# Optimization experiments

Measured on AMD Instinct MI355X. Metric: run time of the kernel, lower is better.

The kernel has to match this reference:

```python
import jax, jax.numpy as jnp
import numpy as np

S = 32            # state_size
K = 26            # neighbors
N_LOCAL, N_FUNC = 3, 14
DT = 0.3          # CNF Euler step size
CNF_STEPS = 3
GATE_H = 8


def _layernorm(x, g, b, eps=1e-5):
    mu = jnp.mean(x, axis=-1, keepdims=True)
    var = jnp.mean((x - mu) ** 2, axis=-1, keepdims=True)
    return (x - mu) * jax.lax.rsqrt(var + eps) * g + b


def setup_inputs() -> dict:
    key = jax.random.key(0)
    ks = jax.random.split(key, 16)
    B = 65536
    def w(k, shape, scale=0.1):
        return jax.random.normal(k, shape, dtype=jnp.float32) * scale
    return {
        "current_state": jax.random.normal(ks[0], (B, S), dtype=jnp.float32),
        "neighbor_states": jax.random.normal(ks[1], (B, K, S), dtype=jnp.float32),
        # local expert (SimpleLinear): [state, mean(local_nb)] -> state
        "Wl": w(ks[2], (2 * S, S)), "bl": jnp.zeros((S,), jnp.float32),
        # functional expert (hybrid GNN + CNF)
        "Wm": w(ks[3], (S, S)), "bm": jnp.zeros((S,), jnp.float32),
        "Wu": w(ks[4], (2 * S, S)), "bu": jnp.zeros((S,), jnp.float32),
        "Wc": w(ks[5], (S, S)), "bc": jnp.zeros((S,), jnp.float32),
        # distant expert (lightweight CNF)
        "Wd": w(ks[6], (2 * S, S)), "bd": jnp.zeros((S,), jnp.float32),
        # gating network
        "ln_g": jnp.ones((S,), jnp.float32), "ln_b": jnp.zeros((S,), jnp.float32),
        "gW1": w(ks[7], (2 * S, GATE_H)), "gb1": jnp.zeros((GATE_H,), jnp.float32),
        "gW2": w(ks[8], (GATE_H, 3)), "gb2": jnp.zeros((3,), jnp.float32),
    }


def reference(current_state, neighbor_states, Wl, bl, Wm, bm, Wu, bu, Wc, bc,
              Wd, bd, ln_g, ln_b, gW1, gb1, gW2, gb2):
    x = current_state                                   # [B, S]
    # --- tier classification (static slices per connection_ratios) ---
    nb_local = neighbor_states[:, :N_LOCAL]             # [B, 3, S]
    nb_func = neighbor_states[:, N_LOCAL:N_LOCAL + N_FUNC]  # [B, 14, S]
    nb_dist = neighbor_states[:, N_LOCAL + N_FUNC:]     # [B, 9, S]

    # --- local expert: simple linear on [state, mean(local neighbors)] ---
    loc_agg = jnp.mean(nb_local, axis=1)
    y_local = x + jnp.tanh(jnp.concatenate([x, loc_agg], -1) @ Wl + bl)

    # --- functional expert: GNN message passing + one CNF Euler step ---
    msgs = jax.nn.gelu(nb_func @ Wm + bm)               # [B, 14, S]
    agg = jnp.mean(msgs, axis=1)                        # [B, S]
    h = x + jnp.tanh(jnp.concatenate([x, agg], -1) @ Wu + bu)
    y_func = h + DT * jnp.tanh(h @ Wc + bc)

    # --- distant expert: lightweight CNF (Euler integration) ---
    dist_agg = jnp.mean(nb_dist, axis=1)                # [B, S]
    xt = x
    for _ in range(CNF_STEPS):
        xt = xt + DT * jnp.tanh(jnp.concatenate([xt, dist_agg], -1) @ Wd + bd)
    y_dist = xt

    # --- gating network (exact GatingNetwork math) ---
    neighbor_activity = jnp.mean(jnp.abs(neighbor_states), axis=1)  # [B, S]
    ctx = jnp.concatenate([_layernorm(x, ln_g, ln_b), neighbor_activity], -1)
    gate = jax.nn.softmax(jax.nn.gelu(ctx @ gW1 + gb1) @ gW2 + gb2, axis=-1)  # [B, 3]

    stacked = jnp.stack([y_local, y_func, y_dist], axis=1)  # [B, 3, S]
    combined = jnp.sum(stacked * gate[..., None], axis=1)   # [B, S]
    return combined, gate
```

## Files before the change

kernel.cpp:

```cpp
#include <hip/hip_runtime.h>

typedef float f32x4 __attribute__((ext_vector_type(4)));
typedef __bf16 bf16x8 __attribute__((ext_vector_type(8)));
typedef unsigned short ushort8 __attribute__((ext_vector_type(8)));

#define S 32
#define DTC 0.3f

__device__ __forceinline__ float frcp(float x) { return __builtin_amdgcn_rcpf(x); }

__device__ __forceinline__ float ftanh(float x) {
    float e = __expf(2.0f * x);
    return 1.0f - 2.0f * frcp(e + 1.0f);
}

__device__ __forceinline__ float fgelu(float x) {
    float t = ftanh(0.7978845608028654f * x * (1.0f + 0.044715f * x * x));
    return 0.5f * x * (1.0f + t);
}

__device__ __forceinline__ unsigned short f2bf(float f) {
    unsigned int u = __builtin_bit_cast(unsigned int, f);
    u += 0x7fffu + ((u >> 16) & 1u);
    return (unsigned short)(u >> 16);
}

union ABFrag { ushort8 u; bf16x8 v; };

__device__ __forceinline__ void load_row8(const float* p, float out[8]) {
    const float4* q = reinterpret_cast<const float4*>(p);
    float4 a = q[0], b = q[1];
    out[0]=a.x; out[1]=a.y; out[2]=a.z; out[3]=a.w;
    out[4]=b.x; out[5]=b.y; out[6]=b.z; out[7]=b.w;
}

__device__ __forceinline__ ABFrag pack8(const float f[8]) {
    ABFrag r;
    #pragma unroll
    for (int e = 0; e < 8; e++) r.u[e] = f2bf(f[e]);
    return r;
}

__device__ __forceinline__ ABFrag load_w(const float* W, int kbase, int col) {
    ABFrag r;
    #pragma unroll
    for (int e = 0; e < 8; e++) r.u[e] = f2bf(W[(kbase + e) * S + col]);
    return r;
}

#define MFMA(a, b, c) __builtin_amdgcn_mfma_f32_16x16x32_bf16((a), (b), (c), 0, 0, 0)

#define BOUNCE(dstFrag, srcC, scale)                                            \
    {                                                                           \
        _Pragma("unroll")                                                       \
        for (int nt_ = 0; nt_ < 2; nt_++)                                       \
            _Pragma("unroll")                                                   \
            for (int r_ = 0; r_ < 4; r_++)                                      \
                lbuf[wid][(4*lg + r_)*40 + lr + 16*nt_] =                       \
                    f2bf((srcC)[nt_][r_] * (scale));                            \
        __syncthreads();                                                        \
        (dstFrag).u = *(const ushort8*)&lbuf[wid][lr*40 + 8*lg];                \
        __syncthreads();                                                        \
    }

__global__ __launch_bounds__(256, 1) void moe_kernel(
    const float* __restrict__ cs,  const float* __restrict__ nb,
    const float* __restrict__ Wl,  const float* __restrict__ bl,
    const float* __restrict__ Wm,  const float* __restrict__ bm,
    const float* __restrict__ Wu,  const float* __restrict__ bu,
    const float* __restrict__ Wc,  const float* __restrict__ bc,
    const float* __restrict__ Wd,  const float* __restrict__ bd,
    const float* __restrict__ lng, const float* __restrict__ lnb,
    const float* __restrict__ gW1, const float* __restrict__ gb1,
    const float* __restrict__ gW2, const float* __restrict__ gb2,
    float* __restrict__ out, int B)
{
    __shared__ __align__(16) unsigned short lbuf[4][16 * 40];
    __shared__ float gbuf[4][16][4];

    const int tid = threadIdx.x;
    const int wid = tid >> 6, lane = tid & 63;
    const int lr = lane & 15, lg = lane >> 4;
    const int b0 = (blockIdx.x * 4 + wid) * 16;
    if (b0 >= B) return;

    ABFrag WlB[2][2], WuB[2][2], WdB[2][2], WmB[2], WcB[2];
    #pragma unroll
    for (int nt = 0; nt < 2; nt++) {
        const int col = lr + 16 * nt;
        #pragma unroll
        for (int kt = 0; kt < 2; kt++) {
            WlB[kt][nt] = load_w(Wl, kt * 32 + 8 * lg, col);
            WuB[kt][nt] = load_w(Wu, kt * 32 + 8 * lg, col);
            WdB[kt][nt] = load_w(Wd, kt * 32 + 8 * lg, col);
        }
        WmB[nt] = load_w(Wm, 8 * lg, col);
        WcB[nt] = load_w(Wc, 8 * lg, col);
    }
    const float blc[2] = { bl[lr], bl[lr + 16] };
    const float bmc[2] = { bm[lr], bm[lr + 16] };
    const float buc[2] = { bu[lr], bu[lr + 16] };
    const float bcc[2] = { bc[lr], bc[lr + 16] };
    const float bdc[2] = { bd[lr], bd[lr + 16] };

    float xf[8];
    load_row8(cs + (size_t)(b0 + lr) * S + 8 * lg, xf);
    ABFrag xA = pack8(xf);
    float xC[2][4];
    #pragma unroll
    for (int nt = 0; nt < 2; nt++)
        #pragma unroll
        for (int r = 0; r < 4; r++)
            xC[nt][r] = cs[(size_t)(b0 + 4 * lg + r) * S + lr + 16 * nt];

    float act[8];
    #pragma unroll
    for (int e = 0; e < 8; e++) act[e] = 0.0f;

    float locf[8];
    #pragma unroll
    for (int e = 0; e < 8; e++) locf[e] = 0.0f;
    #pragma unroll
    for (int k = 0; k < 3; k++) {
        float rf[8];
        load_row8(nb + ((size_t)(b0 + lr) * 26 + k) * S + 8 * lg, rf);
        #pragma unroll
        for (int e = 0; e < 8; e++) { locf[e] += rf[e]; act[e] += fabsf(rf[e]); }
    }
    #pragma unroll
    for (int e = 0; e < 8; e++) locf[e] *= (1.0f / 3.0f);
    ABFrag locA = pack8(locf);

    float ylC[2][4];
    #pragma unroll
    for (int nt = 0; nt < 2; nt++) {
        f32x4 acc = { blc[nt], blc[nt], blc[nt], blc[nt] };
        acc = MFMA(xA.v,   WlB[0][nt].v, acc);
        acc = MFMA(locA.v, WlB[1][nt].v, acc);
        #pragma unroll
        for (int r = 0; r < 4; r++) ylC[nt][r] = xC[nt][r] + ftanh(acc[r]);
    }

    float aggC[2][4];
    #pragma unroll
    for (int nt = 0; nt < 2; nt++)
        #pragma unroll
        for (int r = 0; r < 4; r++) aggC[nt][r] = 0.0f;
    #pragma unroll 2
    for (int k = 0; k < 14; k++) {
        float rf[8];
        load_row8(nb + ((size_t)(b0 + lr) * 26 + 3 + k) * S + 8 * lg, rf);
        #pragma unroll
        for (int e = 0; e < 8; e++) act[e] += fabsf(rf[e]);
        ABFrag a = pack8(rf);
        #pragma unroll
        for (int nt = 0; nt < 2; nt++) {
            f32x4 am = { bmc[nt], bmc[nt], bmc[nt], bmc[nt] };
            am = MFMA(a.v, WmB[nt].v, am);
            #pragma unroll
            for (int r = 0; r < 4; r++) aggC[nt][r] += fgelu(am[r]);
        }
    }

    ABFrag aggA;
    BOUNCE(aggA, aggC, (1.0f / 14.0f));

    float hC[2][4], yfC[2][4];
    #pragma unroll
    for (int nt = 0; nt < 2; nt++) {
        f32x4 acc = { buc[nt], buc[nt], buc[nt], buc[nt] };
        acc = MFMA(xA.v,   WuB[0][nt].v, acc);
        acc = MFMA(aggA.v, WuB[1][nt].v, acc);
        #pragma unroll
        for (int r = 0; r < 4; r++) hC[nt][r] = xC[nt][r] + ftanh(acc[r]);
    }
    ABFrag hA;
    BOUNCE(hA, hC, 1.0f);
    #pragma unroll
    for (int nt = 0; nt < 2; nt++) {
        f32x4 acc = { bcc[nt], bcc[nt], bcc[nt], bcc[nt] };
        acc = MFMA(hA.v, WcB[nt].v, acc);
        #pragma unroll
        for (int r = 0; r < 4; r++) yfC[nt][r] = hC[nt][r] + DTC * ftanh(acc[r]);
    }

    float distf[8];
    #pragma unroll
    for (int e = 0; e < 8; e++) distf[e] = 0.0f;
    #pragma unroll 3
    for (int k = 0; k < 9; k++) {
        float rf[8];
        load_row8(nb + ((size_t)(b0 + lr) * 26 + 17 + k) * S + 8 * lg, rf);
        #pragma unroll
        for (int e = 0; e < 8; e++) { distf[e] += rf[e]; act[e] += fabsf(rf[e]); }
    }
    #pragma unroll
    for (int e = 0; e < 8; e++) distf[e] *= (1.0f / 9.0f);
    ABFrag distA = pack8(distf);

    {
        float s = 0.0f;
        #pragma unroll
        for (int e = 0; e < 8; e++) s += xf[e];
        s += __shfl_xor(s, 16); s += __shfl_xor(s, 32);
        const float mu = s * (1.0f / S);
        float v = 0.0f;
        #pragma unroll
        for (int e = 0; e < 8; e++) { float d = xf[e] - mu; v += d * d; }
        v += __shfl_xor(v, 16); v += __shfl_xor(v, 32);
        const float rstd = rsqrtf(v * (1.0f / S) + 1e-5f);

        float g1v[8];
        #pragma unroll
        for (int u = 0; u < 8; u++) g1v[u] = 0.0f;
        #pragma unroll
        for (int e = 0; e < 8; e++) {
            const int i = 8 * lg + e;
            const float a  = (xf[e] - mu) * rstd * lng[i] + lnb[i];
            const float ac = act[e] * (1.0f / 26.0f);
            #pragma unroll
            for (int u = 0; u < 8; u++)
                g1v[u] += a * gW1[i * 8 + u] + ac * gW1[(S + i) * 8 + u];
        }
        float l0 = gb2[0], l1 = gb2[1], l2 = gb2[2];
        #pragma unroll
        for (int u = 0; u < 8; u++) {
            float gt = g1v[u];
            gt += __shfl_xor(gt, 16); gt += __shfl_xor(gt, 32);
            const float g = fgelu(gt + gb1[u]);
            l0 += g * gW2[u * 3 + 0];
            l1 += g * gW2[u * 3 + 1];
            l2 += g * gW2[u * 3 + 2];
        }
        const float mx = fmaxf(l0, fmaxf(l1, l2));
        const float e0 = __expf(l0 - mx), e1 = __expf(l1 - mx), e2 = __expf(l2 - mx);
        const float rs = frcp(e0 + e1 + e2);
        if (lg == 0) {
            gbuf[wid][lr][0] = e0 * rs;
            gbuf[wid][lr][1] = e1 * rs;
            gbuf[wid][lr][2] = e2 * rs;
        }
    }
    __syncthreads();

    float xtC[2][4];
    #pragma unroll
    for (int nt = 0; nt < 2; nt++)
        #pragma unroll
        for (int r = 0; r < 4; r++) xtC[nt][r] = xC[nt][r];
    ABFrag xtA = xA;
    #pragma unroll 1
    for (int it = 0; it < 3; it++) {
        #pragma unroll
        for (int nt = 0; nt < 2; nt++) {
            f32x4 acc = { bdc[nt], bdc[nt], bdc[nt], bdc[nt] };
            acc = MFMA(xtA.v,  WdB[0][nt].v, acc);
            acc = MFMA(distA.v, WdB[1][nt].v, acc);
            #pragma unroll
            for (int r = 0; r < 4; r++) xtC[nt][r] += DTC * ftanh(acc[r]);
        }
        if (it < 2) { BOUNCE(xtA, xtC, 1.0f); }
    }

    #pragma unroll
    for (int nt = 0; nt < 2; nt++)
        #pragma unroll
        for (int r = 0; r < 4; r++) {
            const int brow = 4 * lg + r;
            const float g0 = gbuf[wid][brow][0];
            const float g1 = gbuf[wid][brow][1];
            const float g2 = gbuf[wid][brow][2];
            out[(size_t)(b0 + brow) * S + lr + 16 * nt] =
                g0 * ylC[nt][r] + g1 * yfC[nt][r] + g2 * xtC[nt][r];
        }
    if (lg == 0) {
        float* gp = out + (size_t)B * S + (size_t)(b0 + lr) * 3;
        gp[0] = gbuf[wid][lr][0];
        gp[1] = gbuf[wid][lr][1];
        gp[2] = gbuf[wid][lr][2];
    }
}

extern "C" void kernel_launch(void* const* d_in, const int* in_sizes, int n_in,
                              void* d_out, int out_size, void* d_ws, size_t ws_size,
                              hipStream_t stream)
{
    const int B = in_sizes[0] / S;
    dim3 block(256);
    dim3 grid((B + 63) / 64);
    hipLaunchKernelGGL(moe_kernel, grid, block, 0, stream,
        (const float*)d_in[0],  (const float*)d_in[1],
        (const float*)d_in[2],  (const float*)d_in[3],
        (const float*)d_in[4],  (const float*)d_in[5],
        (const float*)d_in[6],  (const float*)d_in[7],
        (const float*)d_in[8],  (const float*)d_in[9],
        (const float*)d_in[10], (const float*)d_in[11],
        (const float*)d_in[12], (const float*)d_in[13],
        (const float*)d_in[14], (const float*)d_in[15],
        (const float*)d_in[16], (const float*)d_in[17],
        (float*)d_out, B);
}
```

Baseline: 56.07 us.

## Replace block barriers with wave-local LDS fences and use native bf16 conversion

Each wave only touches its own slice of the LDS bounce and gate buffers, so the block-wide __syncthreads calls become an s_waitcnt lgkmcnt(0) plus a compiler reorder fence. The aim is to stop the four waves stalling on each other. Manual round-to-nearest bf16 packing is replaced by native __bf16 casts. Launch bounds are raised to allow two blocks per CU, and the layernorm and gate weights are now loaded as float4 vectors instead of scalars. The main risk is correctness: this relies on wave-synchronous LDS visibility, and the compiler could reorder LDS accesses around the inline-asm fences.

```diff
diff --git a/kernel.cpp b/kernel.cpp
--- a/kernel.cpp
+++ b/kernel.cpp
@@ -2,7 +2,6 @@
 
 typedef float f32x4 __attribute__((ext_vector_type(4)));
 typedef __bf16 bf16x8 __attribute__((ext_vector_type(8)));
-typedef unsigned short ushort8 __attribute__((ext_vector_type(8)));
 
 #define S 32
 #define DTC 0.3f
@@ -19,13 +18,10 @@
     return 0.5f * x * (1.0f + t);
 }
 
-__device__ __forceinline__ unsigned short f2bf(float f) {
-    unsigned int u = __builtin_bit_cast(unsigned int, f);
-    u += 0x7fffu + ((u >> 16) & 1u);
-    return (unsigned short)(u >> 16);
-}
-
-union ABFrag { ushort8 u; bf16x8 v; };
+#define WAVE_LDS_FENCE() asm volatile("s_waitcnt lgkmcnt(0)" ::: "memory")
+#define REORDER_FENCE()  asm volatile("" ::: "memory")
+
+union ABFrag { bf16x8 v; };
 
 __device__ __forceinline__ void load_row8(const float* p, float out[8]) {
     const float4* q = reinterpret_cast<const float4*>(p);
@@ -37,14 +33,14 @@
 __device__ __forceinline__ ABFrag pack8(const float f[8]) {
     ABFrag r;
     #pragma unroll
-    for (int e = 0; e < 8; e++) r.u[e] = f2bf(f[e]);
+    for (int e = 0; e < 8; e++) r.v[e] = (__bf16)f[e];
     return r;
 }
 
 __device__ __forceinline__ ABFrag load_w(const float* W, int kbase, int col) {
     ABFrag r;
     #pragma unroll
-    for (int e = 0; e < 8; e++) r.u[e] = f2bf(W[(kbase + e) * S + col]);
+    for (int e = 0; e < 8; e++) r.v[e] = (__bf16)W[(kbase + e) * S + col];
     return r;
 }
 
@@ -57,13 +53,13 @@
             _Pragma("unroll")                                                   \
             for (int r_ = 0; r_ < 4; r_++)                                      \
                 lbuf[wid][(4*lg + r_)*40 + lr + 16*nt_] =                       \
-                    f2bf((srcC)[nt_][r_] * (scale));                            \
-        __syncthreads();                                                        \
-        (dstFrag).u = *(const ushort8*)&lbuf[wid][lr*40 + 8*lg];                \
-        __syncthreads();                                                        \
-    }
-
-__global__ __launch_bounds__(256, 1) void moe_kernel(
+                    (__bf16)((srcC)[nt_][r_] * (scale));                        \
+        WAVE_LDS_FENCE();                                                       \
+        (dstFrag).v = *(const bf16x8*)&lbuf[wid][lr*40 + 8*lg];                 \
+        REORDER_FENCE();                                                        \
+    }
+
+__global__ __launch_bounds__(256, 2) void moe_kernel(
     const float* __restrict__ cs,  const float* __restrict__ nb,
     const float* __restrict__ Wl,  const float* __restrict__ bl,
     const float* __restrict__ Wm,  const float* __restrict__ bm,
@@ -75,7 +71,7 @@
     const float* __restrict__ gW2, const float* __restrict__ gb2,
     float* __restrict__ out, int B)
 {
-    __shared__ __align__(16) unsigned short lbuf[4][16 * 40];
+    __shared__ __align__(16) __bf16 lbuf[4][16 * 40];
     __shared__ float gbuf[4][16][4];
 
     const int tid = threadIdx.x;
@@ -210,17 +206,23 @@
         v += __shfl_xor(v, 16); v += __shfl_xor(v, 32);
         const float rstd = rsqrtf(v * (1.0f / S) + 1e-5f);
 
+        float lngv[8], lnbv[8];
+        load_row8(lng + 8 * lg, lngv);
+        load_row8(lnb + 8 * lg, lnbv);
+
         float g1v[8];
         #pragma unroll
         for (int u = 0; u < 8; u++) g1v[u] = 0.0f;
         #pragma unroll
         for (int e = 0; e < 8; e++) {
             const int i = 8 * lg + e;
-            const float a  = (xf[e] - mu) * rstd * lng[i] + lnb[i];
+            const float a  = (xf[e] - mu) * rstd * lngv[e] + lnbv[e];
             const float ac = act[e] * (1.0f / 26.0f);
+            float w1[8], w2[8];
+            load_row8(gW1 + i * 8, w1);
+            load_row8(gW1 + (S + i) * 8, w2);
             #pragma unroll
-            for (int u = 0; u < 8; u++)
-                g1v[u] += a * gW1[i * 8 + u] + ac * gW1[(S + i) * 8 + u];
+            for (int u = 0; u < 8; u++) g1v[u] += a * w1[u] + ac * w2[u];
         }
         float l0 = gb2[0], l1 = gb2[1], l2 = gb2[2];
         #pragma unroll
@@ -240,8 +242,8 @@
             gbuf[wid][lr][1] = e1 * rs;
             gbuf[wid][lr][2] = e2 * rs;
         }
-    }
-    __syncthreads();
+        WAVE_LDS_FENCE();
+    }
 
     float xtC[2][4];
     #pragma unroll
```

Result: faster. 49.49 us (-11.7%).
